# Optimization experiments

Measured on AMD Instinct MI355X. Metric: run time of the kernel, lower is better.

The kernel has to match this reference:

```python
import jax, jax.numpy as jnp
import numpy as np

MIN_NODES = 30
MAX_DEPTH = 8
N = 65536
FMAP = 64


def _kernel(A, B):
    # Gaussian RBF between all row pairs: A [n,f], B [m,f] -> [n,m]
    d2 = (jnp.sum(A * A, -1)[:, None] + jnp.sum(B * B, -1)[None, :]
          - 2.0 * (A @ B.T))
    return jnp.exp(-d2 / A.shape[-1])


def _dfs(X, depth):
    """X: [n, f]. Returns (all_nodes [m,f], indices np[2,nnz], list-of-value-chunks).
    Recursion depth/branching depends only on static shapes -> jit compatible."""
    n = X.shape[0]
    if n <= MIN_NODES or depth == MAX_DEPTH:
        # dense leaf: cartesian-product kernel, row-major flatten matches
        # (repeat-each, tile) ordering of the torch _cartesian
        v = _kernel(X, X).reshape(-1)                       # [n*n]
        r = np.arange(n)
        i = np.stack([np.repeat(r, n), np.tile(r, n)])      # [2, n*n]
        return X, i, [v]
    # midpoint split (concrete _divide)
    l_nodes, l_i, l_v = _dfs(X[: n // 2], depth + 1)
    r_nodes, r_i, r_v = _dfs(X[n // 2:], depth + 1)
    r_i = r_i + l_nodes.shape[0]
    all_nodes = jnp.concatenate([l_nodes, r_nodes], 0)      # [m, f]
    m = all_nodes.shape[0]
    new_node = jnp.mean(all_nodes, 0, keepdims=True)        # [1, f]
    new_v = _kernel(all_nodes, new_node)[:, 0]              # [m]
    ar = np.arange(m)
    full = np.full(m, m)
    new_i = np.concatenate([np.stack([ar, full]),
                            np.stack([full, ar]),
                            np.array([[m], [m]])], 1)       # [2, 2m+1]
    i = np.concatenate([l_i, r_i, new_i], 1)
    vs = l_v + r_v + [new_v, new_v, jnp.ones((1,), X.dtype)]
    return jnp.concatenate([all_nodes, new_node], 0), i, vs


def setup_inputs() -> dict:
    key = jax.random.key(0)
    X = jax.random.normal(key, (1, N, FMAP), dtype=jnp.float32)
    return {"X": X}


def reference(X):
    nodes, idx, vs = _dfs(X[0], depth=1)
    all_nodes = nodes[None]                                 # [1, total, f]
    indices = jnp.asarray(idx, dtype=jnp.int32)             # [2, nnz] COO
    values = jnp.concatenate(vs)                            # [nnz]
    return (all_nodes, indices, values)
```

## Files before the change

### kernel.cpp

```cpp
#include <hip/hip_runtime.h>
#include <hip/hip_bf16.h>
#include <stdint.h>

#define NNZ       34473347LL
#define IDX0_OFF  4202432LL
#define IDX1_OFF  38675779LL
#define VALS_OFF  73149126LL
#define OUT_TOTAL 107622473LL

typedef float f4a __attribute__((ext_vector_type(4), aligned(4)));

__constant__ int       cN[9] = {0, 65663, 32831, 16415, 8207, 4103, 2051, 1025, 512};
__constant__ long long cV[9] = {0, 34473347LL, 17171011LL, 8552675LL, 4259923LL,
                                2121755LL, 1056775LL, 526337LL, 262144LL};
__constant__ int       cSZ[8] = {0, 131325, 65661, 32829, 16413, 8205, 4101, 2049};
__constant__ int gD[21] = {2, 3,3, 4,4,4, 5,5,5,5, 6,6,6,6,6, 7,7,7,7,7,7};
__constant__ int gA[21] = {1, 1,2, 1,2,3, 1,2,3,4, 1,2,3,4,5, 1,2,3,4,5,6};
__constant__ int gB[21] = {0, 2,6, 10,18,26, 34,50,66,82, 98,130,162,194,226,
                           258,322,386,450,514,578};

#define MB_LEAF  2048
#define MB_INT   2304
#define MB_IDXI  5902
#define MB_NODEL 9998
#define MB_ALL   10191

__global__ void r23_sums(const float* __restrict__ X, float* __restrict__ sums) {
    __shared__ float part[4][64];
    int t = blockIdx.x;
    int k = threadIdx.x & 63, p = threadIdx.x >> 6;
    const float* xp = X + (long long)t * 32768;
    float s = 0.f;
    for (int i = p * 128; i < p * 128 + 128; ++i) s += xp[(long long)i * 64 + k];
    part[p][k] = s;
    __syncthreads();
    if (threadIdx.x < 64)
        sums[t * 64 + k] = part[0][k] + part[1][k] + part[2][k] + part[3][k];
}

__global__ void r23_means(const float* __restrict__ sums, float* __restrict__ means,
                          float* __restrict__ mn2, float* __restrict__ out) {
    int h = blockIdx.x + 1;
    int k = threadIdx.x;
    int d = 32 - __clz(h);
    int t = h - (1 << (d - 1));
    int lo = t << (8 - d), cnt = 1 << (8 - d);
    float s = 0.f;
    for (int l = lo; l < lo + cnt; ++l) s += sums[l * 64 + k];
    float mv = s / (float)(1 << (17 - d));
    means[blockIdx.x * 64 + k] = mv;
    long long bb = 0;
    for (int jj = 1; jj <= d - 1; ++jj)
        if ((t >> (d - 1 - jj)) & 1) bb += cN[jj + 1];
    out[(bb + cN[d] - 1) * 64 + k] = mv;
    float sq = mv * mv;
    #pragma unroll
    for (int o = 32; o; o >>= 1) sq += __shfl_xor(sq, o, 64);
    if (k == 0) mn2[blockIdx.x] = sq;
}

__global__ __launch_bounds__(256, 4) void r23_main(const float* __restrict__ X,
                                                   const float* __restrict__ means,
                                                   const float* __restrict__ mn2,
                                                   float* __restrict__ out) {
    __shared__ float As[32][128];
    __shared__ float Bs[32][128];
    int bid = blockIdx.x;
    int tid = threadIdx.x;

    if (bid < MB_LEAF) {
        int t = bid >> 4, tile = bid & 15, br = tile >> 2, bc = tile & 3;
        long long voff = 0; int nb = 0;
        #pragma unroll
        for (int jj = 1; jj <= 7; ++jj)
            if ((t >> (7 - jj)) & 1) { voff += cV[jj + 1]; nb += cN[jj + 1]; }
        const float* xleaf = X + (long long)t * 32768;

        float acc[8][8] = {};
        float na[8] = {}, nb2[8] = {};
        for (int ks = 0; ks < 64; ks += 32) {
            __syncthreads();
            #pragma unroll
            for (int u = 0; u < 4; ++u) {
                int idx = tid * 4 + u;
                int i = idx >> 3, k4 = (idx & 7) * 4;
                float4 va = *(const float4*)&xleaf[(long long)(br * 128 + i) * 64 + ks + k4];
                As[k4 + 0][i] = va.x; As[k4 + 1][i] = va.y; As[k4 + 2][i] = va.z; As[k4 + 3][i] = va.w;
                float4 vb = *(const float4*)&xleaf[(long long)(bc * 128 + i) * 64 + ks + k4];
                Bs[k4 + 0][i] = vb.x; Bs[k4 + 1][i] = vb.y; Bs[k4 + 2][i] = vb.z; Bs[k4 + 3][i] = vb.w;
            }
            __syncthreads();
            int ty = tid >> 4, tx = tid & 15;
            for (int k = 0; k < 32; ++k) {
                float a[8], bb[8];
                *(float4*)&a[0]  = *(const float4*)&As[k][ty * 8];
                *(float4*)&a[4]  = *(const float4*)&As[k][ty * 8 + 4];
                *(float4*)&bb[0] = *(const float4*)&Bs[k][tx * 4];
                *(float4*)&bb[4] = *(const float4*)&Bs[k][64 + tx * 4];
                #pragma unroll
                for (int r = 0; r < 8; ++r)
                    #pragma unroll
                    for (int c = 0; c < 8; ++c) acc[r][c] += a[r] * bb[c];
                #pragma unroll
                for (int r = 0; r < 8; ++r) na[r] = fmaf(a[r], a[r], na[r]);
                #pragma unroll
                for (int c = 0; c < 8; ++c) nb2[c] = fmaf(bb[c], bb[c], nb2[c]);
            }
        }

        int ty = tid >> 4, tx = tid & 15;
        int r0g = br * 128 + ty * 8;
        int cga = bc * 128 + tx * 4;

        f4a i1q[2];
        #pragma unroll
        for (int c = 0; c < 4; ++c) {
            i1q[0][c] = (float)(nb + cga + c);
            i1q[1][c] = (float)(nb + cga + 64 + c);
        }

        #pragma unroll
        for (int r = 0; r < 8; ++r) {
            int grow = r0g + r;
            float nar = na[r];
            float i0f = (float)(nb + grow);
            f4a i0q = {i0f, i0f, i0f, i0f};
            long long rb = voff + (long long)grow * 512;
            #pragma unroll
            for (int h = 0; h < 2; ++h) {
                long long cb = rb + cga + h * 64;
                f4a vv;
                #pragma unroll
                for (int c = 0; c < 4; ++c) {
                    float d2 = nar + nb2[h * 4 + c] - 2.0f * acc[r][h * 4 + c];
                    vv[c] = __expf(-d2 * 0.015625f);
                }
                *(f4a*)&out[VALS_OFF + cb] = vv;
                *(f4a*)&out[IDX0_OFF + cb] = i0q;
                *(f4a*)&out[IDX1_OFF + cb] = i1q[h];
            }
        }
    } else if (bid < MB_INT) {
        int r = ((bid - MB_LEAF) << 8) + tid;
        float4 xv[16];
        const float4* xp = (const float4*)(X + (long long)r * 64);
        #pragma unroll
        for (int i = 0; i < 16; ++i) xv[i] = xp[i];
        float xnr = 0.f;
        #pragma unroll
        for (int i = 0; i < 16; ++i)
            xnr += xv[i].x * xv[i].x + xv[i].y * xv[i].y
                 + xv[i].z * xv[i].z + xv[i].w * xv[i].w;
        int t7 = r >> 9, col = r & 511;
        long long voff = 0;
        #pragma unroll
        for (int d = 1; d <= 7; ++d) {
            int h0 = (1 << (d - 1)) + (r >> (17 - d)) - 1;
            const float* mrow = means + h0 * 64;
            float dot = 0.f;
            #pragma unroll
            for (int i = 0; i < 16; ++i)
                dot += xv[i].x * mrow[4 * i] + xv[i].y * mrow[4 * i + 1]
                     + xv[i].z * mrow[4 * i + 2] + xv[i].w * mrow[4 * i + 3];
            long long q = col;
            #pragma unroll
            for (int jj = 1; jj <= 7; ++jj)
                if (jj >= d && ((t7 >> (7 - jj)) & 1)) q += cN[jj + 1];
            long long m = cN[d] - 1;
            long long co = voff + 2 * cV[d + 1];
            float v = __expf(-(xnr - 2.0f * dot + mn2[h0]) * 0.015625f);
            out[VALS_OFF + co + q]     = v;
            out[VALS_OFF + co + m + q] = v;
            if ((t7 >> (7 - d)) & 1) voff += cV[d + 1];
        }
    } else if (bid < MB_IDXI) {
        int local = bid - MB_INT;
        int d = local / 514 + 1;
        int bx = local % 514;
        int sz = cSZ[d];
        int m = cN[d] - 1;
        long long pos = (long long)bx * 256 + tid;
        long long tot = (long long)(1 << (d - 1)) * sz;
        if (pos < tot) {
            int t = (int)(pos / sz);
            int e = (int)(pos % sz);
            long long voff = 0; long long base = 0;
            for (int jj = 1; jj < d; ++jj)
                if ((t >> (d - 1 - jj)) & 1) { voff += cV[jj + 1]; base += cN[jj + 1]; }
            long long p = voff + 2 * cV[d + 1] + e;
            long long i0, i1;
            if (e < m)          { i0 = base + e;     i1 = base + m; }
            else if (e < 2 * m) { i0 = base + m;     i1 = base + e - m; }
            else                { i0 = base + m;     i1 = base + m; }
            out[IDX0_OFF + p] = (float)i0;
            out[IDX1_OFF + p] = (float)i1;
        }
    } else if (bid < MB_NODEL) {
        int local = bid - MB_IDXI;
        long long e = ((long long)local * 256 + tid) * 4;
        int t = (int)(e >> 15);
        int l = (int)(e & 32767);
        int j = l >> 6, k = l & 63;
        int b = 0;
        #pragma unroll
        for (int jj = 1; jj <= 7; ++jj) if ((t >> (7 - jj)) & 1) b += cN[jj + 1];
        float4 v = *(const float4*)&X[e];
        *(float4*)&out[((long long)b + j) * 64 + k] = v;
    } else {
        int local = bid - MB_NODEL;
        int wv = (local << 2) + (tid >> 6);
        int lane = tid & 63;
        if (wv >= 769) return;
        if (wv < 642) {
            int g = 0;
            while (g < 20 && wv >= gB[g + 1]) ++g;
            int dp = gD[g], a = gA[g];
            int tp = wv - gB[g];
            int hp = (1 << (dp - 1)) + tp;
            int ha = hp >> (dp - a);
            float da = means[(hp - 1) * 64 + lane] - means[(ha - 1) * 64 + lane];
            float s = da * da;
            #pragma unroll
            for (int o = 32; o; o >>= 1) s += __shfl_xor(s, o, 64);
            if (lane == 0) {
                float v = __expf(-s * 0.015625f);
                int ta = ha - (1 << (a - 1));
                long long voff = 0;
                for (int jj = 1; jj <= a - 1; ++jj)
                    if ((ta >> (a - 1 - jj)) & 1) voff += cV[jj + 1];
                long long q = cN[dp] - 1;
                for (int jj = a; jj <= dp - 1; ++jj)
                    if ((tp >> (dp - 1 - jj)) & 1) q += cN[jj + 1];
                long long m = cN[a] - 1;
                long long co = voff + 2 * cV[a + 1];
                out[VALS_OFF + co + q]     = v;
                out[VALS_OFF + co + m + q] = v;
            }
        } else if (lane == 0) {
            int h = wv - 642 + 1;
            int d = 32 - __clz(h);
            int t = h - (1 << (d - 1));
            long long voff = 0;
            for (int jj = 1; jj <= d - 1; ++jj)
                if ((t >> (d - 1 - jj)) & 1) voff += cV[jj + 1];
            long long m = cN[d] - 1;
            out[VALS_OFF + voff + 2 * cV[d + 1] + 2 * m] = 1.0f;
        }
    }
}

extern "C" void kernel_launch(void* const* d_in, const int* in_sizes, int n_in,
                              void* d_out, int out_size, void* d_ws, size_t ws_size,
                              hipStream_t stream) {
    const float* X = (const float*)d_in[0];
    float* out = (float*)d_out;

    float* sums  = (float*)d_ws;
    float* means = sums + 128 * 64;
    float* mn2   = means + 127 * 64;

    if (out_size != (int)OUT_TOTAL) return;
    if (ws_size < (size_t)(128 * 64 + 127 * 64 + 128) * sizeof(float)) return;

    r23_sums <<<128,    256, 0, stream>>>(X, sums);
    r23_means<<<127,     64, 0, stream>>>(sums, means, mn2, out);
    r23_main <<<MB_ALL, 256, 0, stream>>>(X, means, mn2, out);
}
```

Baseline: 215.4 us.

## Exploit leaf kernel symmetry: compute upper-triangle tiles and write transposes

Leaf Gram tiles are now computed only for the 10 upper-triangular tile pairs out of 16 per leaf. Off-diagonal tiles are transposed through shared memory and written a second time as the mirrored block. This cuts GEMM work and X reloads for leaves by roughly 37%. In exchange it adds extra syncs, a shared-memory transpose, and heavier per-block work, and it drops the occupancy hint from launch bounds. The kernel is write-bound, so total store traffic stays unchanged.

```diff
diff --git a/kernel.cpp b/kernel.cpp
--- a/kernel.cpp
+++ b/kernel.cpp
@@ -18,14 +18,16 @@
 __constant__ int gA[21] = {1, 1,2, 1,2,3, 1,2,3,4, 1,2,3,4,5, 1,2,3,4,5,6};
 __constant__ int gB[21] = {0, 2,6, 10,18,26, 34,50,66,82, 98,130,162,194,226,
                            258,322,386,450,514,578};
-
-#define MB_LEAF  2048
-#define MB_INT   2304
-#define MB_IDXI  5902
-#define MB_NODEL 9998
-#define MB_ALL   10191
-
-__global__ void r23_sums(const float* __restrict__ X, float* __restrict__ sums) {
+__constant__ int tBR[10] = {0,0,0,0,1,1,1,2,2,3};
+__constant__ int tBC[10] = {0,1,2,3,1,2,3,2,3,3};
+
+#define MB_LEAF  1280
+#define MB_INT   1536
+#define MB_IDXI  5134
+#define MB_NODEL 9230
+#define MB_ALL   9423
+
+__global__ void r24_sums(const float* __restrict__ X, float* __restrict__ sums) {
     __shared__ float part[4][64];
     int t = blockIdx.x;
     int k = threadIdx.x & 63, p = threadIdx.x >> 6;
@@ -38,7 +40,7 @@
         sums[t * 64 + k] = part[0][k] + part[1][k] + part[2][k] + part[3][k];
 }
 
-__global__ void r23_means(const float* __restrict__ sums, float* __restrict__ means,
+__global__ void r24_means(const float* __restrict__ sums, float* __restrict__ means,
                           float* __restrict__ mn2, float* __restrict__ out) {
     int h = blockIdx.x + 1;
     int k = threadIdx.x;
@@ -59,17 +61,20 @@
     if (k == 0) mn2[blockIdx.x] = sq;
 }
 
-__global__ __launch_bounds__(256, 4) void r23_main(const float* __restrict__ X,
-                                                   const float* __restrict__ means,
-                                                   const float* __restrict__ mn2,
-                                                   float* __restrict__ out) {
-    __shared__ float As[32][128];
-    __shared__ float Bs[32][128];
+__global__ __launch_bounds__(256) void r24_main(const float* __restrict__ X,
+                                                const float* __restrict__ means,
+                                                const float* __restrict__ mn2,
+                                                float* __restrict__ out) {
+    __shared__ __align__(16) char shbuf[64 * 132 * 4];
+    float (*As)[128] = (float (*)[128])shbuf;
+    float (*Bs)[128] = (float (*)[128])(shbuf + 16384);
+    float (*T)[132]  = (float (*)[132])shbuf;
     int bid = blockIdx.x;
     int tid = threadIdx.x;
 
     if (bid < MB_LEAF) {
-        int t = bid >> 4, tile = bid & 15, br = tile >> 2, bc = tile & 3;
+        int t = bid / 10, u = bid - t * 10;
+        int br = tBR[u], bc = tBC[u];
         long long voff = 0; int nb = 0;
         #pragma unroll
         for (int jj = 1; jj <= 7; ++jj)
@@ -81,8 +86,8 @@
         for (int ks = 0; ks < 64; ks += 32) {
             __syncthreads();
             #pragma unroll
-            for (int u = 0; u < 4; ++u) {
-                int idx = tid * 4 + u;
+            for (int uu = 0; uu < 4; ++uu) {
+                int idx = tid * 4 + uu;
                 int i = idx >> 3, k4 = (idx & 7) * 4;
                 float4 va = *(const float4*)&xleaf[(long long)(br * 128 + i) * 64 + ks + k4];
                 As[k4 + 0][i] = va.x; As[k4 + 1][i] = va.y; As[k4 + 2][i] = va.z; As[k4 + 3][i] = va.w;
@@ -138,6 +143,37 @@
                 *(f4a*)&out[VALS_OFF + cb] = vv;
                 *(f4a*)&out[IDX0_OFF + cb] = i0q;
                 *(f4a*)&out[IDX1_OFF + cb] = i1q[h];
+            }
+        }
+
+        if (br != bc) {
+            for (int h = 0; h < 2; ++h) {
+                __syncthreads();
+                #pragma unroll
+                for (int r = 0; r < 8; ++r)
+                    #pragma unroll
+                    for (int c = 0; c < 4; ++c) {
+                        float d2 = na[r] + nb2[h * 4 + c] - 2.0f * acc[r][h * 4 + c];
+                        T[tx * 4 + c][ty * 8 + r] = __expf(-d2 * 0.015625f);
+                    }
+                __syncthreads();
+                int i = tid >> 2, seg = tid & 3;
+                int rowl = bc * 128 + h * 64 + i;
+                long long base = voff + (long long)rowl * 512 + br * 128 + seg * 32;
+                float i0f2 = (float)(nb + rowl);
+                f4a i0q2 = {i0f2, i0f2, i0f2, i0f2};
+                #pragma unroll
+                for (int j4 = 0; j4 < 8; ++j4) {
+                    f4a vq, i1v2;
+                    #pragma unroll
+                    for (int c = 0; c < 4; ++c) {
+                        vq[c]  = T[i][seg * 32 + j4 * 4 + c];
+                        i1v2[c] = (float)(nb + br * 128 + seg * 32 + j4 * 4 + c);
+                    }
+                    *(f4a*)&out[VALS_OFF + base + j4 * 4] = vq;
+                    *(f4a*)&out[IDX0_OFF + base + j4 * 4] = i0q2;
+                    *(f4a*)&out[IDX1_OFF + base + j4 * 4] = i1v2;
+                }
             }
         }
     } else if (bid < MB_INT) {
@@ -262,7 +298,7 @@
     if (out_size != (int)OUT_TOTAL) return;
     if (ws_size < (size_t)(128 * 64 + 127 * 64 + 128) * sizeof(float)) return;
 
-    r23_sums <<<128,    256, 0, stream>>>(X, sums);
-    r23_means<<<127,     64, 0, stream>>>(sums, means, mn2, out);
-    r23_main <<<MB_ALL, 256, 0, stream>>>(X, means, mn2, out);
+    r24_sums <<<128,    256, 0, stream>>>(X, sums);
+    r24_means<<<127,     64, 0, stream>>>(sums, means, mn2, out);
+    r24_main <<<MB_ALL, 256, 0, stream>>>(X, means, mn2, out);
 }
```

Result: slower. 268.1 us (+24.5%).
